# Kernel optimization log

Hardware: AMD Instinct MI355X
Metric: run time of the kernel (lower is better)

## Reference

```python
import jax, jax.numpy as jnp
import numpy as np

MUL = 32                      # multiplicity of every irrep in in1/out (uvu: mul_in1 == mul_out)
DIMS = (1, 3, 5)              # irrep dims for l = 0, 1, 2
Z = 400000                    # batch (e.g. number of edges)
# all (l1, l2, l3) paths allowed by the triangle inequality -> 15 instructions
INS = [(i1, i2, i3) for i1 in range(3) for i2 in range(3) for i3 in range(3)
       if abs(i1 - i2) <= i3 <= i1 + i2]
D1 = MUL * sum(DIMS)          # 288, flattened in1 feature dim
D2 = sum(DIMS)                # 9,  flattened in2 feature dim (mul=1)
OFF1 = np.concatenate([[0], np.cumsum([MUL * d for d in DIMS])])  # block offsets in x1
OFF2 = np.concatenate([[0], np.cumsum(DIMS)])                     # block offsets in x2
MAXD = max(DIMS)


def setup_inputs() -> dict:
    key = jax.random.key(0)
    k1, k2, k3 = jax.random.split(key, 3)
    x1 = jax.random.normal(k1, (Z, D1), dtype=jnp.float32)
    x2 = jax.random.normal(k2, (Z, D2), dtype=jnp.float32)
    # stand-in Clebsch-Gordan tensors, padded to [n_ins, 5, 5, 5]; only the
    # [:d1, :d2, :d3] block of path p is ever read.
    cg = jax.random.normal(k3, (len(INS), MAXD, MAXD, MAXD), dtype=jnp.float32)
    return {"x1": x1, "x2": x2, "cg": cg}


def reference(x1, x2, cg):
    z = x1.shape[0]
    # split into per-irrep blocks: x1 -> [z, mul, dim], x2 -> [z, 1, dim]
    x1b = [x1[:, OFF1[i]:OFF1[i + 1]].reshape(z, MUL, DIMS[i]) for i in range(3)]
    x2b = [x2[:, OFF2[i]:OFF2[i + 1]].reshape(z, 1, DIMS[i]) for i in range(3)]
    acc = [jnp.zeros((z, MUL * d), dtype=x1.dtype) for d in DIMS]
    for p, (i1, i2, i3) in enumerate(INS):
        d1, d2, d3 = DIMS[i1], DIMS[i2], DIMS[i3]
        cgp = cg[p, :d1, :d2, :d3]
        # uvu, unweighted: torch.einsum('ijk,zuvij->zuk', cg, einsum('zui,zvj->zuvij', x1, x2))
        # fused (avoids the zuvij intermediate); path_weight = 1.0
        res = jnp.einsum('ijk,zui,zvj->zuk', cgp, x1b[i1], x2b[i2])
        acc[i3] = acc[i3] + res.reshape(z, MUL * d3)
    return jnp.concatenate(acc, axis=1)  # [z, 288]
```

## Files before the change

### kernel.cpp

```cpp
#include <hip/hip_runtime.h>


namespace {
constexpr int kZ    = 400000;
constexpr int kMul  = 32;
constexpr int kDims[3] = {1, 3, 5};
constexpr int kCOff[3] = {0, 1, 4};
}

__global__ __launch_bounds__(256) void tp_kernel(
    const float* __restrict__ x1,
    const float* __restrict__ x2,
    const float* __restrict__ cg,
    float* __restrict__ out)
{
    const int g = blockIdx.x * blockDim.x + threadIdx.x;
    const int u = g & (kMul - 1);
    const int z = g >> 5;
    if (z >= kZ) return;

    const float* __restrict__ x1r = x1 + (size_t)z * 288;
    const float* __restrict__ x2r = x2 + (size_t)z * 9;

    float a[9], b[9], o[9];

    a[0] = x1r[u];
#pragma unroll
    for (int m = 0; m < 3; ++m) a[1 + m] = x1r[32 + u * 3 + m];
#pragma unroll
    for (int m = 0; m < 5; ++m) a[4 + m] = x1r[128 + u * 5 + m];

#pragma unroll
    for (int j = 0; j < 9; ++j) b[j] = x2r[j];

#pragma unroll
    for (int k = 0; k < 9; ++k) o[k] = 0.0f;

#define DO_INS(P, I1, I2, I3)                                                  \
    {                                                                          \
        constexpr int d1 = kDims[I1], d2 = kDims[I2], d3 = kDims[I3];          \
        constexpr int s1 = kCOff[I1], s2 = kCOff[I2], s3 = kCOff[I3];          \
        _Pragma("unroll")                                                      \
        for (int i = 0; i < d1; ++i) {                                         \
            _Pragma("unroll")                                                  \
            for (int j = 0; j < d2; ++j) {                                     \
                const float pij = a[s1 + i] * b[s2 + j];                       \
                _Pragma("unroll")                                              \
                for (int k = 0; k < d3; ++k) {                                 \
                    o[s3 + k] = fmaf(cg[(P) * 125 + i * 25 + j * 5 + k], pij,  \
                                     o[s3 + k]);                               \
                }                                                              \
            }                                                                  \
        }                                                                      \
    }

    DO_INS(0,  0, 0, 0)
    DO_INS(1,  0, 1, 1)
    DO_INS(2,  0, 2, 2)
    DO_INS(3,  1, 0, 1)
    DO_INS(4,  1, 1, 0)
    DO_INS(5,  1, 1, 1)
    DO_INS(6,  1, 1, 2)
    DO_INS(7,  1, 2, 1)
    DO_INS(8,  1, 2, 2)
    DO_INS(9,  2, 0, 2)
    DO_INS(10, 2, 1, 1)
    DO_INS(11, 2, 1, 2)
    DO_INS(12, 2, 2, 0)
    DO_INS(13, 2, 2, 1)
    DO_INS(14, 2, 2, 2)
#undef DO_INS

    float* __restrict__ outr = out + (size_t)z * 288;
    outr[u] = o[0];
#pragma unroll
    for (int k = 0; k < 3; ++k) outr[32 + u * 3 + k] = o[1 + k];
#pragma unroll
    for (int k = 0; k < 5; ++k) outr[128 + u * 5 + k] = o[4 + k];
}

extern "C" void kernel_launch(void* const* d_in, const int* in_sizes, int n_in,
                              void* d_out, int out_size, void* d_ws, size_t ws_size,
                              hipStream_t stream) {
    const float* x1 = (const float*)d_in[0];
    const float* x2 = (const float*)d_in[1];
    const float* cg = (const float*)d_in[2];
    float* out = (float*)d_out;

    const int total = kZ * kMul;
    const int block = 256;
    const int grid = (total + block - 1) / block;
    tp_kernel<<<grid, block, 0, stream>>>(x1, x2, cg, out);
}
```

Baseline: 761.7 us.

## Precontract CG with x2 per row into shared 9x9 matrix reused across multiplicity lanes

Each block handles 8 batch rows. Per row, it first contracts the CG tensors with the x2 vector into a 9x9 block-sparse matrix stored in shared memory, using a constexpr index table. Every multiplicity lane then does a dense 9x9 matvec with its x1 slice. This removes redundant per-lane CG-times-x2 products and most per-thread FMAs, at the cost of two block barriers and LDS traffic.

```diff
diff --git a/kernel.cpp b/kernel.cpp
--- a/kernel.cpp
+++ b/kernel.cpp
@@ -2,74 +2,106 @@
 
 
 namespace {
-constexpr int kZ    = 400000;
-constexpr int kMul  = 32;
-constexpr int kDims[3] = {1, 3, 5};
-constexpr int kCOff[3] = {0, 1, 4};
+constexpr int kZ     = 400000;
+constexpr int kZTile = 8;
+constexpr int kBlock = 256;
+
+struct Tab { int v[81 * 3]; };
+
+constexpr int blk_of(int g) { return (g >= 1) + (g >= 4); }
+
+constexpr Tab make_tab() {
+    Tab t{};
+    const int ins[15][3] = {
+        {0,0,0},{0,1,1},{0,2,2},{1,0,1},{1,1,0},{1,1,1},{1,1,2},{1,2,1},
+        {1,2,2},{2,0,2},{2,1,1},{2,1,2},{2,2,0},{2,2,1},{2,2,2}};
+    int pidx[27];
+    for (int x = 0; x < 27; ++x) pidx[x] = -1;
+    for (int p = 0; p < 15; ++p)
+        pidx[ins[p][0] * 9 + ins[p][1] * 3 + ins[p][2]] = p;
+    const int goff[3] = {0, 1, 4};
+    for (int i = 0; i < 9; ++i)
+        for (int k = 0; k < 9; ++k)
+            for (int i2 = 0; i2 < 3; ++i2) {
+                const int bi = blk_of(i), bk = blk_of(k);
+                const int p  = pidx[bi * 9 + i2 * 3 + bk];
+                t.v[(i * 9 + k) * 3 + i2] =
+                    (p < 0) ? -1
+                            : p * 125 + (i - goff[bi]) * 25 + (k - goff[bk]);
+            }
+    return t;
 }
 
-__global__ __launch_bounds__(256) void tp_kernel(
+__device__ const Tab kTab = make_tab();
+}
+
+__global__ __launch_bounds__(kBlock) void tp_kernel(
     const float* __restrict__ x1,
     const float* __restrict__ x2,
     const float* __restrict__ cg,
     float* __restrict__ out)
 {
-    const int g = blockIdx.x * blockDim.x + threadIdx.x;
-    const int u = g & (kMul - 1);
-    const int z = g >> 5;
-    if (z >= kZ) return;
+    __shared__ float x2s[kZTile * 9];
+    __shared__ float Ws[kZTile][9][12];
+
+    const int tid = threadIdx.x;
+    const int u   = tid & 31;
+    const int zl  = tid >> 5;
+    const int z   = blockIdx.x * kZTile + zl;
 
     const float* __restrict__ x1r = x1 + (size_t)z * 288;
-    const float* __restrict__ x2r = x2 + (size_t)z * 9;
-
-    float a[9], b[9], o[9];
-
+    float a[9];
     a[0] = x1r[u];
 #pragma unroll
     for (int m = 0; m < 3; ++m) a[1 + m] = x1r[32 + u * 3 + m];
 #pragma unroll
     for (int m = 0; m < 5; ++m) a[4 + m] = x1r[128 + u * 5 + m];
 
+    if (tid < kZTile * 9) x2s[tid] = x2[(size_t)blockIdx.x * kZTile * 9 + tid];
+    __syncthreads();
+
+    float xb[9];
 #pragma unroll
-    for (int j = 0; j < 9; ++j) b[j] = x2r[j];
+    for (int j = 0; j < 9; ++j) xb[j] = x2s[zl * 9 + j];
 
+    for (int r = u; r < 81; r += 32) {
+        const int i = r / 9;
+        const int k = r - i * 9;
+        const int* tp = &kTab.v[r * 3];
+        float w = 0.0f;
+        {
+            const int b = tp[0];
+            if (b >= 0) w = fmaf(cg[b], xb[0], w);
+        }
+        {
+            const int b = tp[1];
+            if (b >= 0) {
+#pragma unroll
+                for (int lj = 0; lj < 3; ++lj)
+                    w = fmaf(cg[b + 5 * lj], xb[1 + lj], w);
+            }
+        }
+        {
+            const int b = tp[2];
+            if (b >= 0) {
+#pragma unroll
+                for (int lj = 0; lj < 5; ++lj)
+                    w = fmaf(cg[b + 5 * lj], xb[4 + lj], w);
+            }
+        }
+        Ws[zl][i][k] = w;
+    }
+    __syncthreads();
+
+    float o[9];
 #pragma unroll
     for (int k = 0; k < 9; ++k) o[k] = 0.0f;
-
-#define DO_INS(P, I1, I2, I3)                                                  \
-    {                                                                          \
-        constexpr int d1 = kDims[I1], d2 = kDims[I2], d3 = kDims[I3];          \
-        constexpr int s1 = kCOff[I1], s2 = kCOff[I2], s3 = kCOff[I3];          \
-        _Pragma("unroll")                                                      \
-        for (int i = 0; i < d1; ++i) {                                         \
-            _Pragma("unroll")                                                  \
-            for (int j = 0; j < d2; ++j) {                                     \
-                const float pij = a[s1 + i] * b[s2 + j];                       \
-                _Pragma("unroll")                                              \
-                for (int k = 0; k < d3; ++k) {                                 \
-                    o[s3 + k] = fmaf(cg[(P) * 125 + i * 25 + j * 5 + k], pij,  \
-                                     o[s3 + k]);                               \
-                }                                                              \
-            }                                                                  \
-        }                                                                      \
+#pragma unroll
+    for (int i = 0; i < 9; ++i) {
+#pragma unroll
+        for (int k = 0; k < 9; ++k)
+            o[k] = fmaf(a[i], Ws[zl][i][k], o[k]);
     }
-
-    DO_INS(0,  0, 0, 0)
-    DO_INS(1,  0, 1, 1)
-    DO_INS(2,  0, 2, 2)
-    DO_INS(3,  1, 0, 1)
-    DO_INS(4,  1, 1, 0)
-    DO_INS(5,  1, 1, 1)
-    DO_INS(6,  1, 1, 2)
-    DO_INS(7,  1, 2, 1)
-    DO_INS(8,  1, 2, 2)
-    DO_INS(9,  2, 0, 2)
-    DO_INS(10, 2, 1, 1)
-    DO_INS(11, 2, 1, 2)
-    DO_INS(12, 2, 2, 0)
-    DO_INS(13, 2, 2, 1)
-    DO_INS(14, 2, 2, 2)
-#undef DO_INS
 
     float* __restrict__ outr = out + (size_t)z * 288;
     outr[u] = o[0];
@@ -87,8 +119,6 @@
     const float* cg = (const float*)d_in[2];
     float* out = (float*)d_out;
 
-    const int total = kZ * kMul;
-    const int block = 256;
-    const int grid = (total + block - 1) / block;
-    tp_kernel<<<grid, block, 0, stream>>>(x1, x2, cg, out);
+    const int grid = kZ / kZTile;
+    tp_kernel<<<grid, kBlock, 0, stream>>>(x1, x2, cg, out);
 }
```

After: 873.0 us. +14.6%, slower.
